# Performance work log

Hardware: AMD Instinct MI355X
Metric: run time of the kernel (lower is better)

The kernel has to match this reference:

```python
import jax, jax.numpy as jnp
import numpy as np

B, N, D, H = 4, 1024, 512, 8
DH = D // H  # per-head dim for V and for each of the two Q/K halves
LAM = 0.5


def setup_inputs() -> dict:
    key = jax.random.key(0)
    ks = jax.random.split(key, 7)
    s = 0.02
    return {
        "x": jax.random.normal(ks[0], (B, N, D), dtype=jnp.float32),
        "Wq": jax.random.normal(ks[1], (D, 2 * D), dtype=jnp.float32) * s,
        "bq": jax.random.normal(ks[2], (2 * D,), dtype=jnp.float32) * s,
        "Wk": jax.random.normal(ks[3], (D, 2 * D), dtype=jnp.float32) * s,
        "bk": jax.random.normal(ks[4], (2 * D,), dtype=jnp.float32) * s,
        "Wv": jax.random.normal(ks[5], (D, D), dtype=jnp.float32) * s,
        "bv": jax.random.normal(ks[6], (D,), dtype=jnp.float32) * s,
    }


def reference(x, Wq, bq, Wk, bk, Wv, bv):
    b, n, d = x.shape
    q = (x @ Wq + bq).reshape(b, n, H, 2 * DH).transpose(0, 2, 1, 3)  # [B,H,N,2*DH]
    k = (x @ Wk + bk).reshape(b, n, H, 2 * DH).transpose(0, 2, 1, 3)
    v = (x @ Wv + bv).reshape(b, n, H, DH).transpose(0, 2, 1, 3)      # [B,H,N,DH]
    q1, q2 = q[..., :DH], q[..., DH:]
    k1, k2 = k[..., :DH], k[..., DH:]
    scale = 1.0 / jnp.sqrt(jnp.float32(DH))
    a1 = jax.nn.softmax(jnp.einsum("bhqd,bhkd->bhqk", q1, k1) * scale, axis=-1)
    a2 = jax.nn.softmax(jnp.einsum("bhqd,bhkd->bhqk", q2, k2) * scale, axis=-1)
    attn = a1 - LAM * a2                                              # [B,H,N,N]
    out = jnp.einsum("bhqk,bhkd->bhqd", attn, v)                      # [B,H,N,DH]
    return out.transpose(0, 2, 1, 3).reshape(b, n, d)
```

## Files before the change

### kernel.cpp

```cpp
#include <hip/hip_runtime.h>
#include <hip/hip_bf16.h>

typedef unsigned short u16;
typedef unsigned int u32;
typedef short s16x8 __attribute__((ext_vector_type(8)));
typedef short s16x4 __attribute__((ext_vector_type(4)));
typedef float f32x4 __attribute__((ext_vector_type(4)));

__device__ inline u16 f2bf(float f) {
  union { float f; unsigned int u; } v; v.f = f;
  unsigned int r = v.u + 0x7fffu + ((v.u >> 16) & 1u);
  return (u16)(r >> 16);
}

__device__ __forceinline__ u32 cvt_pk_bf16(float lo, float hi) {
  u32 r;
  asm("v_cvt_pk_bf16_f32 %0, %1, %2" : "=v"(r) : "v"(lo), "v"(hi));
  return r;
}

__device__ __forceinline__ void g2lds16(const u16* g, u16* l) {
  __builtin_amdgcn_global_load_lds((const __attribute__((address_space(1))) void*)g,
                                   (__attribute__((address_space(3))) void*)l, 16, 0, 0);
}

__global__ __launch_bounds__(256) void cast_x_kernel(const float* __restrict__ x,
                                                     u16* __restrict__ xb) {
  int i = (blockIdx.x * 256 + threadIdx.x) * 8;
  float4 a = *(const float4*)(x + i);
  float4 b = *(const float4*)(x + i + 4);
  s16x8 o;
  o[0] = (short)f2bf(a.x); o[1] = (short)f2bf(a.y);
  o[2] = (short)f2bf(a.z); o[3] = (short)f2bf(a.w);
  o[4] = (short)f2bf(b.x); o[5] = (short)f2bf(b.y);
  o[6] = (short)f2bf(b.z); o[7] = (short)f2bf(b.w);
  *(s16x8*)(xb + i) = o;
}

__global__ __launch_bounds__(256) void transpose_cast_w_all(const float* __restrict__ Wq,
                                                            const float* __restrict__ Wk,
                                                            const float* __restrict__ Wv,
                                                            u16* __restrict__ wt) {
  __shared__ float tile[64][65];
  int jg = blockIdx.x * 64;
  const float* src; int C, j0;
  if (jg < 1024)      { src = Wq; C = 1024; j0 = jg; }
  else if (jg < 2048) { src = Wk; C = 1024; j0 = jg - 1024; }
  else                { src = Wv; C = 512;  j0 = jg - 2048; }
  int k0 = blockIdx.y * 64;
  int tx = threadIdx.x % 64, ty4 = threadIdx.x / 64;
#pragma unroll
  for (int p = 0; p < 16; ++p) {
    int r = p * 4 + ty4;
    tile[r][tx] = src[(size_t)(k0 + r) * C + j0 + tx];
  }
  __syncthreads();
#pragma unroll
  for (int p = 0; p < 16; ++p) {
    int r = p * 4 + ty4;
    wt[(size_t)(jg + r) * 512 + k0 + tx] = f2bf(tile[tx][r]);
  }
}

__global__ __launch_bounds__(256, 2) void gemm_qkv(const u16* __restrict__ xb, const u16* __restrict__ wt,
                                                   const float* __restrict__ bq, const float* __restrict__ bk,
                                                   const float* __restrict__ bv,
                                                   u16* __restrict__ qa, u16* __restrict__ ka,
                                                   u16* __restrict__ va) {
  __shared__ __align__(16) u16 As[128 * 64];
  __shared__ __align__(16) u16 Bs[128 * 64];
  int m0 = blockIdx.x * 128, j0 = blockIdx.y * 128;
  int tid = threadIdx.x;
  int w = tid >> 6, lane = tid & 63, quad = lane >> 4, l16 = lane & 15;
  int wr = (w >> 1) * 64, wc = (w & 1) * 64;

  int srow[4], scol[4], sbase[4];
#pragma unroll
  for (int it = 0; it < 4; ++it) {
    int s = it * 256 + tid;
    srow[it] = s >> 3;
    scol[it] = (s & 7) ^ ((s >> 3) & 7);
    sbase[it] = (s & ~63) * 8;
  }

  f32x4 acc[4][4];
#pragma unroll
  for (int i = 0; i < 4; ++i)
#pragma unroll
    for (int j = 0; j < 4; ++j)
#pragma unroll
      for (int r = 0; r < 4; ++r) acc[i][j][r] = 0.f;

  for (int kk = 0; kk < 8; ++kk) {
    int k0 = kk * 64;
    __syncthreads();
#pragma unroll
    for (int it = 0; it < 4; ++it) {
      g2lds16(xb + (size_t)(m0 + srow[it]) * 512 + k0 + scol[it] * 8, &As[sbase[it]]);
      g2lds16(wt + (size_t)(j0 + srow[it]) * 512 + k0 + scol[it] * 8, &Bs[sbase[it]]);
    }
    __syncthreads();
#pragma unroll
    for (int kb = 0; kb < 2; ++kb) {
      s16x8 af[4], bfr[4];
#pragma unroll
      for (int rb = 0; rb < 4; ++rb) {
        int row = wr + rb * 16 + l16;
        af[rb] = *(const s16x8*)(&As[row * 64 + (((kb * 4 + quad) ^ (row & 7)) * 8)]);
      }
#pragma unroll
      for (int cb = 0; cb < 4; ++cb) {
        int row = wc + cb * 16 + l16;
        bfr[cb] = *(const s16x8*)(&Bs[row * 64 + (((kb * 4 + quad) ^ (row & 7)) * 8)]);
      }
#pragma unroll
      for (int rb = 0; rb < 4; ++rb)
#pragma unroll
        for (int cb = 0; cb < 4; ++cb)
          acc[rb][cb] = __builtin_amdgcn_mfma_f32_16x16x32_bf16(af[rb], bfr[cb], acc[rb][cb], 0, 0, 0);
    }
  }

#pragma unroll
  for (int cb = 0; cb < 4; ++cb) {
    int j = j0 + wc + cb * 16 + l16;
    float bias = (j < 1024) ? bq[j] : (j < 2048) ? bk[j - 1024] : bv[j - 2048];
#pragma unroll
    for (int rb = 0; rb < 4; ++rb) {
#pragma unroll
      for (int r = 0; r < 4; ++r) {
        int m = m0 + wr + rb * 16 + quad * 4 + r;
        int bidx = m >> 10, n = m & 1023;
        u16 o = f2bf(acc[rb][cb][r] + bias);
        if (j < 1024) {
          int h = j >> 7, r2 = j & 127;
          qa[((size_t)((bidx * 8 + h) * 1024 + n)) * 128 + r2] = o;
        } else if (j < 2048) {
          int jj = j - 1024, h = jj >> 7, r2 = jj & 127;
          ka[((size_t)((bidx * 8 + h) * 1024 + n)) * 128 + r2] = o;
        } else {
          int jj = j - 2048, h = jj >> 6, d = jj & 63;
          va[((size_t)((bidx * 8 + h) * 64 + d)) * 1024 + n] = o;
        }
      }
    }
  }
}

__global__ __launch_bounds__(512, 4) void attn_kernel(const u16* __restrict__ qa, const u16* __restrict__ ka,
                                                      const u16* __restrict__ va, float* __restrict__ out) {
  __shared__ __align__(16) u16 smem[40960];
  int bh = blockIdx.x, b = bh >> 3, h = bh & 7;
  int q0 = blockIdx.y * 64;
  int tid = threadIdx.x, w = tid >> 6, lane = tid & 63, quad = lane >> 4, l16 = lane & 15;
  int hfid = w >> 2, lw = w & 3, t256 = tid & 255;
  u16* hb = smem + hfid * 20480;
  u16* const KbA = hb;
  u16* const KbB = hb + 8192;
  u16* const Vsb = hb + 16384;

  const u16* qrow = qa + (size_t)(bh * 1024 + q0 + lw * 16 + l16) * 128;
  s16x8 qf[2][2];
  qf[0][0] = *(const s16x8*)(qrow + quad * 8);
  qf[0][1] = *(const s16x8*)(qrow + 32 + quad * 8);
  qf[1][0] = *(const s16x8*)(qrow + 64 + quad * 8);
  qf[1][1] = *(const s16x8*)(qrow + 96 + quad * 8);

  f32x4 O1[5], O2[5];
#pragma unroll
  for (int i = 0; i < 5; ++i)
#pragma unroll
    for (int r = 0; r < 4; ++r) { O1[i][r] = 0.f; O2[i][r] = 0.f; }

  s16x8 onesf;
#pragma unroll
  for (int i = 0; i < 8; ++i) onesf[i] = (l16 == 0) ? (short)0x3F80 : (short)0;

  int krow[4], kcol[4], kbse[4];
#pragma unroll
  for (int it = 0; it < 4; ++it) {
    int s = it * 256 + t256;
    krow[it] = s >> 4; kcol[it] = (s & 15) ^ ((s >> 4) & 7); kbse[it] = (s & ~63) * 8;
  }
  int vrow[2], vcol[2], vbse[2];
#pragma unroll
  for (int it = 0; it < 2; ++it) {
    int s = it * 256 + t256;
    vrow[it] = s >> 3; vcol[it] = (s & 7) ^ ((s >> 3) & 7); vbse[it] = (s & ~63) * 8;
  }
  const u16* kgbase = ka + (size_t)bh * 1024 * 128;
  const u16* vgbase = va + (size_t)bh * 64 * 1024;
  int nbase = hfid * 512;

  auto stageK = [&](int n0, u16* Kd) {
#pragma unroll
    for (int it = 0; it < 4; ++it)
      g2lds16(kgbase + (size_t)(n0 + krow[it]) * 128 + kcol[it] * 8, Kd + kbse[it]);
  };
  auto stageV = [&](int n0) {
#pragma unroll
    for (int it = 0; it < 2; ++it)
      g2lds16(vgbase + (size_t)vrow[it] * 1024 + n0 + vcol[it] * 8, Vsb + vbse[it]);
  };

  stageK(nbase, KbA);
  stageV(nbase);
  __syncthreads();

  for (int kt = 0; kt < 8; ++kt) {
    u16* const KsC = (kt & 1) ? KbB : KbA;
    u16* const KsN = (kt & 1) ? KbA : KbB;
    if (kt < 7) stageK(nbase + (kt + 1) * 64, KsN);

    f32x4 sv[2][4];
#pragma unroll
    for (int hh = 0; hh < 2; ++hh)
#pragma unroll
      for (int nt = 0; nt < 4; ++nt) {
        f32x4 a; a[0] = a[1] = a[2] = a[3] = 0.f;
#pragma unroll
        for (int kb = 0; kb < 2; ++kb) {
          int row = nt * 16 + l16;
          s16x8 kf = *(const s16x8*)(&KsC[row * 128 + (((hh * 8 + kb * 4 + quad) ^ (row & 7)) * 8)]);
          a = __builtin_amdgcn_mfma_f32_16x16x32_bf16(kf, qf[hh][kb], a, 0, 0, 0);
        }
        sv[hh][nt] = a;
      }

    s16x8 vB[4][2];
#pragma unroll
    for (int ct = 0; ct < 4; ++ct) {
      int row = ct * 16 + l16, rx = row & 7;
#pragma unroll
      for (int hf = 0; hf < 2; ++hf) {
        union { s16x4 hl[2]; s16x8 v; } u;
#pragma unroll
        for (int j = 0; j < 2; ++j) {
          int nt = 2 * hf + j;
          int lc = 2 * nt + (quad >> 1);
          u.hl[j] = *(const s16x4*)(&Vsb[row * 64 + (((lc ^ rx) << 3) + ((quad & 1) << 2))]);
        }
        vB[ct][hf] = u.v;
      }
    }

    asm volatile("s_waitcnt lgkmcnt(0)\n\ts_barrier" ::: "memory");
    if (kt < 7) stageV(nbase + (kt + 1) * 64);

    s16x8 pA[2][2];
#pragma unroll
    for (int hh = 0; hh < 2; ++hh)
#pragma unroll
      for (int hf = 0; hf < 2; ++hf) {
        union { u32 wd[4]; s16x8 v; } u;
#pragma unroll
        for (int j = 0; j < 2; ++j) {
          int nt = 2 * hf + j;
          float e0 = __builtin_exp2f(sv[hh][nt][0] * 0.18033688f);
          float e1 = __builtin_exp2f(sv[hh][nt][1] * 0.18033688f);
          float e2 = __builtin_exp2f(sv[hh][nt][2] * 0.18033688f);
          float e3 = __builtin_exp2f(sv[hh][nt][3] * 0.18033688f);
          u.wd[2 * j]     = cvt_pk_bf16(e0, e1);
          u.wd[2 * j + 1] = cvt_pk_bf16(e2, e3);
        }
        pA[hh][hf] = u.v;
      }

#pragma unroll
    for (int ct = 0; ct < 5; ++ct)
#pragma unroll
      for (int hf = 0; hf < 2; ++hf) {
        s16x8 bf = (ct < 4) ? vB[ct][hf] : onesf;
        O1[ct] = __builtin_amdgcn_mfma_f32_16x16x32_bf16(pA[0][hf], bf, O1[ct], 0, 0, 0);
        O2[ct] = __builtin_amdgcn_mfma_f32_16x16x32_bf16(pA[1][hf], bf, O2[ct], 0, 0, 0);
      }

    __syncthreads();
  }

  float* scr = (float*)smem;
  if (w >= 4) {
    int base = (w - 4) * 2560 + lane * 4;
#pragma unroll
    for (int i = 0; i < 5; ++i) {
      *(f32x4*)&scr[base + i * 256]       = O1[i];
      *(f32x4*)&scr[base + (i + 5) * 256] = O2[i];
    }
  }
  __syncthreads();
  if (w < 4) {
    int base = w * 2560 + lane * 4;
#pragma unroll
    for (int i = 0; i < 5; ++i) {
      O1[i] += *(const f32x4*)&scr[base + i * 256];
      O2[i] += *(const f32x4*)&scr[base + (i + 5) * 256];
    }
    float inv1[4], inv2[4];
#pragma unroll
    for (int r = 0; r < 4; ++r) {
      float l1 = __shfl(O1[4][r], lane & 48, 64);
      float l2 = __shfl(O2[4][r], lane & 48, 64);
      inv1[r] = 1.0f / l1;
      inv2[r] = 1.0f / l2;
    }
    int nb = q0 + w * 16 + quad * 4;
#pragma unroll
    for (int ct = 0; ct < 4; ++ct)
#pragma unroll
      for (int r = 0; r < 4; ++r) {
        float val = O1[ct][r] * inv1[r] - 0.5f * O2[ct][r] * inv2[r];
        out[(size_t)(b * 1024 + nb + r) * 512 + h * 64 + ct * 16 + l16] = val;
      }
  }
}

extern "C" void kernel_launch(void* const* d_in, const int* in_sizes, int n_in,
                              void* d_out, int out_size, void* d_ws, size_t ws_size,
                              hipStream_t stream) {
  (void)in_sizes; (void)n_in; (void)out_size; (void)ws_size;
  const float* x  = (const float*)d_in[0];
  const float* Wq = (const float*)d_in[1];
  const float* bq = (const float*)d_in[2];
  const float* Wk = (const float*)d_in[3];
  const float* bk = (const float*)d_in[4];
  const float* Wv = (const float*)d_in[5];
  const float* bv = (const float*)d_in[6];
  float* out = (float*)d_out;

  char* ws = (char*)d_ws;
  u16* xb = (u16*)(ws);
  u16* wt = (u16*)(ws + 4194304);
  u16* qa = (u16*)(ws + 6815744);
  u16* ka = (u16*)(ws + 15204352);
  u16* va = (u16*)(ws + 23592960);

  cast_x_kernel<<<1024, 256, 0, stream>>>(x, xb);
  transpose_cast_w_all<<<dim3(40, 8), 256, 0, stream>>>(Wq, Wk, Wv, wt);
  gemm_qkv<<<dim3(32, 20), 256, 0, stream>>>(xb, wt, bq, bk, bv, qa, ka, va);
  attn_kernel<<<dim3(32, 16), 512, 0, stream>>>(qa, ka, va, out);
}
```

Before: 147.9 us.

## Switch attention kernel to 32x32x16 MFMA tiles with 256-thread blocks

```diff
diff --git a/kernel.cpp b/kernel.cpp
--- a/kernel.cpp
+++ b/kernel.cpp
@@ -6,6 +6,7 @@
 typedef short s16x8 __attribute__((ext_vector_type(8)));
 typedef short s16x4 __attribute__((ext_vector_type(4)));
 typedef float f32x4 __attribute__((ext_vector_type(4)));
+typedef float f32x16 __attribute__((ext_vector_type(16)));
 
 __device__ inline u16 f2bf(float f) {
   union { float f; unsigned int u; } v; v.f = f;
@@ -147,60 +148,52 @@
   }
 }
 
-__global__ __launch_bounds__(512, 4) void attn_kernel(const u16* __restrict__ qa, const u16* __restrict__ ka,
+__global__ __launch_bounds__(256, 2) void attn_kernel(const u16* __restrict__ qa, const u16* __restrict__ ka,
                                                       const u16* __restrict__ va, float* __restrict__ out) {
   __shared__ __align__(16) u16 smem[40960];
   int bh = blockIdx.x, b = bh >> 3, h = bh & 7;
   int q0 = blockIdx.y * 64;
-  int tid = threadIdx.x, w = tid >> 6, lane = tid & 63, quad = lane >> 4, l16 = lane & 15;
-  int hfid = w >> 2, lw = w & 3, t256 = tid & 255;
-  u16* hb = smem + hfid * 20480;
+  int tid = threadIdx.x, w = tid >> 6, lane = tid & 63;
+  int l32 = lane & 31, hi = lane >> 5;
+  int team = w >> 1, wq = w & 1, t = tid & 127;
+  u16* hb = smem + team * 20480;
   u16* const KbA = hb;
   u16* const KbB = hb + 8192;
   u16* const Vsb = hb + 16384;
 
-  const u16* qrow = qa + (size_t)(bh * 1024 + q0 + lw * 16 + l16) * 128;
-  s16x8 qf[2][2];
-  qf[0][0] = *(const s16x8*)(qrow + quad * 8);
-  qf[0][1] = *(const s16x8*)(qrow + 32 + quad * 8);
-  qf[1][0] = *(const s16x8*)(qrow + 64 + quad * 8);
-  qf[1][1] = *(const s16x8*)(qrow + 96 + quad * 8);
-
-  f32x4 O1[5], O2[5];
-#pragma unroll
-  for (int i = 0; i < 5; ++i)
-#pragma unroll
-    for (int r = 0; r < 4; ++r) { O1[i][r] = 0.f; O2[i][r] = 0.f; }
-
-  s16x8 onesf;
-#pragma unroll
-  for (int i = 0; i < 8; ++i) onesf[i] = (l16 == 0) ? (short)0x3F80 : (short)0;
-
-  int krow[4], kcol[4], kbse[4];
-#pragma unroll
-  for (int it = 0; it < 4; ++it) {
-    int s = it * 256 + t256;
-    krow[it] = s >> 4; kcol[it] = (s & 15) ^ ((s >> 4) & 7); kbse[it] = (s & ~63) * 8;
-  }
-  int vrow[2], vcol[2], vbse[2];
-#pragma unroll
-  for (int it = 0; it < 2; ++it) {
-    int s = it * 256 + t256;
-    vrow[it] = s >> 3; vcol[it] = (s & 7) ^ ((s >> 3) & 7); vbse[it] = (s & ~63) * 8;
-  }
+  const u16* qrow = qa + (size_t)(bh * 1024 + q0 + wq * 32 + l32) * 128;
+  s16x8 qf[2][4];
+#pragma unroll
+  for (int hh = 0; hh < 2; ++hh)
+#pragma unroll
+    for (int kb = 0; kb < 4; ++kb)
+      qf[hh][kb] = *(const s16x8*)(qrow + 64 * hh + 16 * kb + 8 * hi);
+
+  f32x16 O1[2], O2[2];
+#pragma unroll
+  for (int d = 0; d < 2; ++d)
+#pragma unroll
+    for (int r = 0; r < 16; ++r) { O1[d][r] = 0.f; O2[d][r] = 0.f; }
+  float ds1 = 0.f, ds2 = 0.f;
+
+  int r0 = t >> 4, c0 = t & 15;
+  int rv = t >> 3, cv = (t & 7) ^ ((t >> 3) & 7);
   const u16* kgbase = ka + (size_t)bh * 1024 * 128;
   const u16* vgbase = va + (size_t)bh * 64 * 1024;
-  int nbase = hfid * 512;
+  int nbase = team * 512;
 
   auto stageK = [&](int n0, u16* Kd) {
 #pragma unroll
-    for (int it = 0; it < 4; ++it)
-      g2lds16(kgbase + (size_t)(n0 + krow[it]) * 128 + kcol[it] * 8, Kd + kbse[it]);
+    for (int it = 0; it < 8; ++it) {
+      int row = r0 + 8 * it;
+      int chunk = c0 ^ (row & 15);
+      g2lds16(kgbase + (size_t)(n0 + row) * 128 + chunk * 8, Kd + (it * 128 + (t & 64)) * 8);
+    }
   };
   auto stageV = [&](int n0) {
 #pragma unroll
-    for (int it = 0; it < 2; ++it)
-      g2lds16(vgbase + (size_t)vrow[it] * 1024 + n0 + vcol[it] * 8, Vsb + vbse[it]);
+    for (int it = 0; it < 4; ++it)
+      g2lds16(vgbase + (size_t)(rv + 16 * it) * 1024 + n0 + cv * 8, Vsb + (it * 128 + (t & 64)) * 8);
   };
 
   stageK(nbase, KbA);
@@ -212,105 +205,105 @@
     u16* const KsN = (kt & 1) ? KbA : KbB;
     if (kt < 7) stageK(nbase + (kt + 1) * 64, KsN);
 
-    f32x4 sv[2][4];
-#pragma unroll
-    for (int hh = 0; hh < 2; ++hh)
-#pragma unroll
-      for (int nt = 0; nt < 4; ++nt) {
-        f32x4 a; a[0] = a[1] = a[2] = a[3] = 0.f;
-#pragma unroll
-        for (int kb = 0; kb < 2; ++kb) {
-          int row = nt * 16 + l16;
-          s16x8 kf = *(const s16x8*)(&KsC[row * 128 + (((hh * 8 + kb * 4 + quad) ^ (row & 7)) * 8)]);
-          a = __builtin_amdgcn_mfma_f32_16x16x32_bf16(kf, qf[hh][kb], a, 0, 0, 0);
+    s16x8 pa[2][4];
+#pragma unroll
+    for (int hh = 0; hh < 2; ++hh) {
+      f32x16 sv[2];
+#pragma unroll
+      for (int nb = 0; nb < 2; ++nb)
+#pragma unroll
+        for (int r = 0; r < 16; ++r) sv[nb][r] = 0.f;
+#pragma unroll
+      for (int nb = 0; nb < 2; ++nb) {
+        int row = nb * 32 + l32, rbase = row * 128, rx15 = row & 15;
+#pragma unroll
+        for (int kb = 0; kb < 4; ++kb) {
+          s16x8 kf = *(const s16x8*)(&KsC[rbase + (((8 * hh + 2 * kb + hi) ^ rx15) * 8)]);
+          sv[nb] = __builtin_amdgcn_mfma_f32_32x32x16_bf16(kf, qf[hh][kb], sv[nb], 0, 0, 0);
         }
-        sv[hh][nt] = a;
-      }
+      }
+      float dsl = 0.f;
+#pragma unroll
+      for (int s = 0; s < 4; ++s) {
+        float e[8];
+#pragma unroll
+        for (int j = 0; j < 8; ++j) {
+          e[j] = __builtin_exp2f(sv[s >> 1][(s & 1) * 8 + j] * 0.18033688f);
+          dsl += e[j];
+        }
+        union { u32 wd[4]; s16x8 v; } u;
+        u.wd[0] = cvt_pk_bf16(e[0], e[1]);
+        u.wd[1] = cvt_pk_bf16(e[2], e[3]);
+        u.wd[2] = cvt_pk_bf16(e[4], e[5]);
+        u.wd[3] = cvt_pk_bf16(e[6], e[7]);
+        pa[hh][s] = u.v;
+      }
+      if (hh == 0) ds1 += dsl; else ds2 += dsl;
+    }
 
     s16x8 vB[4][2];
 #pragma unroll
-    for (int ct = 0; ct < 4; ++ct) {
-      int row = ct * 16 + l16, rx = row & 7;
-#pragma unroll
-      for (int hf = 0; hf < 2; ++hf) {
+    for (int dblk = 0; dblk < 2; ++dblk) {
+      int row = dblk * 32 + l32, rbase = row * 64, rx = row & 7;
+#pragma unroll
+      for (int s = 0; s < 4; ++s) {
         union { s16x4 hl[2]; s16x8 v; } u;
-#pragma unroll
-        for (int j = 0; j < 2; ++j) {
-          int nt = 2 * hf + j;
-          int lc = 2 * nt + (quad >> 1);
-          u.hl[j] = *(const s16x4*)(&Vsb[row * 64 + (((lc ^ rx) << 3) + ((quad & 1) << 2))]);
-        }
-        vB[ct][hf] = u.v;
+        u.hl[0] = *(const s16x4*)(&Vsb[rbase + (((2 * s) ^ rx) * 8) + 4 * hi]);
+        u.hl[1] = *(const s16x4*)(&Vsb[rbase + (((2 * s + 1) ^ rx) * 8) + 4 * hi]);
+        vB[s][dblk] = u.v;
       }
     }
 
     asm volatile("s_waitcnt lgkmcnt(0)\n\ts_barrier" ::: "memory");
     if (kt < 7) stageV(nbase + (kt + 1) * 64);
 
-    s16x8 pA[2][2];
-#pragma unroll
-    for (int hh = 0; hh < 2; ++hh)
-#pragma unroll
-      for (int hf = 0; hf < 2; ++hf) {
-        union { u32 wd[4]; s16x8 v; } u;
-#pragma unroll
-        for (int j = 0; j < 2; ++j) {
-          int nt = 2 * hf + j;
-          float e0 = __builtin_exp2f(sv[hh][nt][0] * 0.18033688f);
-          float e1 = __builtin_exp2f(sv[hh][nt][1] * 0.18033688f);
-          float e2 = __builtin_exp2f(sv[hh][nt][2] * 0.18033688f);
-          float e3 = __builtin_exp2f(sv[hh][nt][3] * 0.18033688f);
-          u.wd[2 * j]     = cvt_pk_bf16(e0, e1);
-          u.wd[2 * j + 1] = cvt_pk_bf16(e2, e3);
-        }
-        pA[hh][hf] = u.v;
-      }
-
-#pragma unroll
-    for (int ct = 0; ct < 5; ++ct)
-#pragma unroll
-      for (int hf = 0; hf < 2; ++hf) {
-        s16x8 bf = (ct < 4) ? vB[ct][hf] : onesf;
-        O1[ct] = __builtin_amdgcn_mfma_f32_16x16x32_bf16(pA[0][hf], bf, O1[ct], 0, 0, 0);
-        O2[ct] = __builtin_amdgcn_mfma_f32_16x16x32_bf16(pA[1][hf], bf, O2[ct], 0, 0, 0);
+#pragma unroll
+    for (int s = 0; s < 4; ++s)
+#pragma unroll
+      for (int dblk = 0; dblk < 2; ++dblk) {
+        O1[dblk] = __builtin_amdgcn_mfma_f32_32x32x16_bf16(pa[0][s], vB[s][dblk], O1[dblk], 0, 0, 0);
+        O2[dblk] = __builtin_amdgcn_mfma_f32_32x32x16_bf16(pa[1][s], vB[s][dblk], O2[dblk], 0, 0, 0);
       }
 
     __syncthreads();
   }
 
   float* scr = (float*)smem;
-  if (w >= 4) {
-    int base = (w - 4) * 2560 + lane * 4;
-#pragma unroll
-    for (int i = 0; i < 5; ++i) {
-      *(f32x4*)&scr[base + i * 256]       = O1[i];
-      *(f32x4*)&scr[base + (i + 5) * 256] = O2[i];
-    }
+  int mbase = wq * 4224 + lane;
+  if (team == 1) {
+#pragma unroll
+    for (int r = 0; r < 16; ++r) {
+      scr[mbase + r * 64]        = O1[0][r];
+      scr[mbase + (16 + r) * 64] = O1[1][r];
+      scr[mbase + (32 + r) * 64] = O2[0][r];
+      scr[mbase + (48 + r) * 64] = O2[1][r];
+    }
+    scr[mbase + 64 * 64] = ds1;
+    scr[mbase + 65 * 64] = ds2;
   }
   __syncthreads();
-  if (w < 4) {
-    int base = w * 2560 + lane * 4;
-#pragma unroll
-    for (int i = 0; i < 5; ++i) {
-      O1[i] += *(const f32x4*)&scr[base + i * 256];
-      O2[i] += *(const f32x4*)&scr[base + (i + 5) * 256];
-    }
-    float inv1[4], inv2[4];
-#pragma unroll
-    for (int r = 0; r < 4; ++r) {
-      float l1 = __shfl(O1[4][r], lane & 48, 64);
-      float l2 = __shfl(O2[4][r], lane & 48, 64);
-      inv1[r] = 1.0f / l1;
-      inv2[r] = 1.0f / l2;
-    }
-    int nb = q0 + w * 16 + quad * 4;
-#pragma unroll
-    for (int ct = 0; ct < 4; ++ct)
-#pragma unroll
-      for (int r = 0; r < 4; ++r) {
-        float val = O1[ct][r] * inv1[r] - 0.5f * O2[ct][r] * inv2[r];
-        out[(size_t)(b * 1024 + nb + r) * 512 + h * 64 + ct * 16 + l16] = val;
-      }
+  if (team == 0) {
+#pragma unroll
+    for (int r = 0; r < 16; ++r) {
+      O1[0][r] += scr[mbase + r * 64];
+      O1[1][r] += scr[mbase + (16 + r) * 64];
+      O2[0][r] += scr[mbase + (32 + r) * 64];
+      O2[1][r] += scr[mbase + (48 + r) * 64];
+    }
+    ds1 += scr[mbase + 64 * 64];
+    ds2 += scr[mbase + 65 * 64];
+    ds1 += __shfl_xor(ds1, 32, 64);
+    ds2 += __shfl_xor(ds2, 32, 64);
+    float inv1 = 1.0f / ds1, inv2 = 1.0f / ds2;
+#pragma unroll
+    for (int r = 0; r < 16; ++r) {
+      int iq = (r & 3) + 8 * (r >> 2) + 4 * hi;
+      float i1 = __shfl(inv1, iq, 64);
+      float i2 = __shfl(inv2, iq, 64);
+      size_t orow = (size_t)(b * 1024 + q0 + wq * 32 + iq) * 512 + h * 64 + l32;
+      out[orow]      = O1[0][r] * i1 - 0.5f * O2[0][r] * i2;
+      out[orow + 32] = O1[1][r] * i1 - 0.5f * O2[1][r] * i2;
+    }
   }
 }
 
@@ -337,5 +330,5 @@
   cast_x_kernel<<<1024, 256, 0, stream>>>(x, xb);
   transpose_cast_w_all<<<dim3(40, 8), 256, 0, stream>>>(Wq, Wk, Wv, wt);
   gemm_qkv<<<dim3(32, 20), 256, 0, stream>>>(xb, wt, bq, bk, bv, qa, ka, va);
-  attn_kernel<<<dim3(32, 16), 512, 0, stream>>>(qa, ka, va, out);
-}
+  attn_kernel<<<dim3(32, 16), 256, 0, stream>>>(qa, ka, va, out);
+}
```

Result: faster. 134.5 us (-9.1%).
